# Performance work log

Measured on AMD Instinct MI355X. Metric: run time of the kernel, lower is better.

The kernel has to match this reference:

```python
import jax, jax.numpy as jnp
import numpy as np

N, E = 50000, 800000
IN = OUT = 128
T, R, H = 4, 6, 8
DK = OUT // H


def setup_inputs() -> dict:
    key = jax.random.key(0)
    ks = iter(jax.random.split(key, 24))
    nk = lambda: next(ks)
    return {
        "node_inp": jax.random.normal(nk(), (N, IN), jnp.float32),
        "node_type": jax.random.randint(nk(), (N,), 0, T),
        "edge_index": jax.random.randint(nk(), (2, E), 0, N),
        "edge_type": jax.random.randint(nk(), (E,), 0, R),
        "edge_sign": jax.random.randint(nk(), (E,), -2, 2),
        "edge_distance": jax.random.uniform(nk(), (E,), jnp.float32, 0.0, 2e5),
        "Wq": jax.random.normal(nk(), (T, IN, OUT), jnp.float32) / np.float32(np.sqrt(IN)),
        "bq": jnp.zeros((T, OUT), jnp.float32),
        "Wk": jax.random.normal(nk(), (T, IN, OUT), jnp.float32) / np.float32(np.sqrt(IN)),
        "bk": jnp.zeros((T, OUT), jnp.float32),
        "Wv": jax.random.normal(nk(), (T, IN, OUT), jnp.float32) / np.float32(np.sqrt(IN)),
        "bv": jnp.zeros((T, OUT), jnp.float32),
        "rel_q": jax.random.normal(nk(), (R, H, DK), jnp.float32) * 0.2,
        "rel_k": jax.random.normal(nk(), (R, H, DK), jnp.float32) * 0.2,
        "rel_v": jax.random.normal(nk(), (R, H, DK), jnp.float32) * 0.2,
        "sign_k_neutral": jnp.ones((H, DK), jnp.float32),
        "sign_v_neutral": jnp.ones((H, DK), jnp.float32),
        "rel_bias": jnp.zeros((R, H), jnp.float32),
        "dist_alpha": jnp.asarray(0.5, jnp.float32),
        "dist_tau": jnp.asarray(100000.0, jnp.float32),
        "skip": jnp.ones((T,), jnp.float32),
        "ln_gamma": jnp.ones((T, OUT), jnp.float32),
        "ln_beta": jnp.zeros((T, OUT), jnp.float32),
    }


def reference(node_inp, node_type, edge_index, edge_type, edge_sign, edge_distance,
              Wq, bq, Wk, bk, Wv, bv, rel_q, rel_k, rel_v,
              sign_k_neutral, sign_v_neutral, rel_bias, dist_alpha, dist_tau,
              skip, ln_gamma, ln_beta):
    n = node_inp.shape[0]
    src, dst = edge_index[0], edge_index[1]

    # edge_sign normalization: anything < -1 or == 0 -> -2 (neutral), else clamp to {-1, 1}
    es = jnp.where((edge_sign < -1) | (edge_sign == 0), -2, jnp.clip(edge_sign, -1, 1))
    sign_idx = jnp.where(es == -1, 0, jnp.where(es == 1, 1, 2))  # [E]

    # per-type Q/K/V projections, then select by node_type
    idx = jnp.arange(n)
    Q = (jnp.einsum('ni,tio->tno', node_inp, Wq) + bq[:, None, :])[node_type, idx]
    K = (jnp.einsum('ni,tio->tno', node_inp, Wk) + bk[:, None, :])[node_type, idx]
    V = (jnp.einsum('ni,tio->tno', node_inp, Wv) + bv[:, None, :])[node_type, idx]
    Q = Q.reshape(n, H, DK); K = K.reshape(n, H, DK); V = V.reshape(n, H, DK)

    sign_k_all = jnp.concatenate([-jnp.ones((1, H, DK), Q.dtype), jnp.ones((1, H, DK), Q.dtype), sign_k_neutral[None]], 0)
    sign_v_all = jnp.concatenate([-jnp.ones((1, H, DK), Q.dtype), jnp.ones((1, H, DK), Q.dtype), sign_v_neutral[None]], 0)

    q_eff = Q[dst] * rel_q[edge_type]                        # [E,H,DK]
    k_eff = K[src] * rel_k[edge_type] * sign_k_all[sign_idx]  # [E,H,DK]
    v_eff = V[src] * rel_v[edge_type] * sign_v_all[sign_idx]  # [E,H,DK]

    scores = (q_eff * k_eff).sum(-1) / np.float32(np.sqrt(DK))  # [E,H]
    scores = scores + rel_bias[edge_type]
    phi = dist_alpha * jnp.exp(-edge_distance / (dist_tau + 1e-9))
    scores = scores + phi[:, None]

    # destination-grouped softmax over edges
    m = jax.ops.segment_max(scores, dst, num_segments=n)      # [N,H]
    ex = jnp.exp(scores - m[dst])
    Z = jax.ops.segment_sum(ex, dst, num_segments=n)          # [N,H]
    attn = ex / (Z[dst] + 1e-9)                               # [E,H]

    msg = (v_eff * attn[..., None]).reshape(-1, OUT)          # [E,OUT]
    out = jax.ops.segment_sum(msg, dst, num_segments=n)       # [N,OUT]

    alpha = jax.nn.sigmoid(skip)[node_type][:, None]          # [N,1]
    mix = alpha * out + (1.0 - alpha) * node_inp
    mu = mix.mean(-1, keepdims=True)
    var = ((mix - mu) ** 2).mean(-1, keepdims=True)
    normed = (mix - mu) / jnp.sqrt(var + 1e-5)
    return normed * ln_gamma[node_type] + ln_beta[node_type]
```

## Files before the change

### kernel.cpp

```cpp
#include <hip/hip_runtime.h>

#define N_NODES 50000
#define N_EDGES 800000
#define DIM 128
#define NT 4
#define NR 6
#define NH 8
#define NBLK_SCAN ((N_NODES + 255) / 256)
#define NBLK2 ((N_NODES + 1023) / 1024)
#define NTILE_ROW 3129
#define NPAD_MAX (NTILE_ROW * 16)

#define XCVT_N (N_NODES * DIM / 4)
#define WT_N   (NT * 3 * DIM * DIM)
#define WCB_N  (24 * 32)
#define PREP_TOTAL (XCVT_N + WT_N + WCB_N)
#define PREP_BLOCKS ((PREP_TOTAL + 255) / 256)
#define HIST_BLOCKS (N_EDGES / 256)
#define A_PREP_BASE NBLK_SCAN
#define A_HIST_BASE (NBLK_SCAN + PREP_BLOCKS)
#define A_BLOCKS (A_HIST_BASE + HIST_BLOCKS)

#define D_BLOCKS 4693

typedef __attribute__((ext_vector_type(8))) short bf16x8;
typedef __attribute__((ext_vector_type(4))) float f32x4;

__device__ __forceinline__ unsigned short f2bf(float f) {
    unsigned int u = __float_as_uint(f);
    return (unsigned short)((u + 0x7fffu + ((u >> 16) & 1u)) >> 16);
}
__device__ __forceinline__ float blo(unsigned int u) { return __uint_as_float(u << 16); }
__device__ __forceinline__ float bhi(unsigned int u) { return __uint_as_float(u & 0xffff0000u); }

__device__ __forceinline__ int sign_index(int s) {
    if (s < -1 || s == 0) return 2;
    return (s == -1) ? 0 : 1;
}

__global__ __launch_bounds__(256) void k_A(
    const int* __restrict__ ntype, int* __restrict__ bhist, int* __restrict__ opad,
    const float* __restrict__ x,
    const float* __restrict__ Wq, const float* __restrict__ Wk, const float* __restrict__ Wv,
    const float* __restrict__ rel_q, const float* __restrict__ rel_k,
    const float* __restrict__ rel_v,
    const float* __restrict__ skn, const float* __restrict__ svn,
    unsigned short* __restrict__ xb, unsigned short* __restrict__ Wt,
    uint4* __restrict__ wcb,
    const int* __restrict__ ei, int* __restrict__ cnt, int* __restrict__ posw)
{
    int blk = blockIdx.x;
    if (blk < NBLK_SCAN) {
        __shared__ int h[NT];
        if (threadIdx.x < NT) h[threadIdx.x] = 0;
        __syncthreads();
        int n = blk * 256 + threadIdx.x;
        if (n < N_NODES) atomicAdd(&h[ntype[n]], 1);
        if (n < NPAD_MAX) opad[n] = -1;
        __syncthreads();
        if (threadIdx.x < NT) bhist[blk * NT + threadIdx.x] = h[threadIdx.x];
        return;
    }
    if (blk < A_HIST_BASE) {
        int i = (blk - A_PREP_BASE) * 256 + threadIdx.x;
        if (i < XCVT_N) {
            float4 v = ((const float4*)x)[i];
            ushort4 o;
            o.x = f2bf(v.x); o.y = f2bf(v.y); o.z = f2bf(v.z); o.w = f2bf(v.w);
            ((ushort4*)xb)[i] = o;
        } else if (i < XCVT_N + WT_N) {
            int j = i - XCVT_N;
            int in = j & 127;
            int b2 = j >> 7;
            int out = b2 & 127;
            int ts = b2 >> 7;
            int sel = ts % 3, t = ts / 3;
            const float* W = sel == 0 ? Wq : (sel == 1 ? Wk : Wv);
            Wt[j] = f2bf(W[((size_t)t * DIM + in) * DIM + out]);
        } else if (i < PREP_TOTAL) {
            int j = i - XCVT_N - WT_N;
            int p = j & 31;
            int cmb = j >> 5;
            int et = cmb & 7, sidx = cmb >> 3;
            if (et < NR) {
                int h2 = p >> 2;
                unsigned d[4];
                #pragma unroll
                for (int q = 0; q < 4; ++q) {
                    int o = 4 * p + q;
                    int rb = (et * NH + h2) * 16 + (o & 15);
                    float sgk = sidx == 0 ? -1.f : (sidx == 1 ? 1.f : skn[o]);
                    float sgv = sidx == 0 ? -1.f : (sidx == 1 ? 1.f : svn[o]);
                    float wk = rel_q[rb] * rel_k[rb] * sgk * 0.25f;
                    float wv = rel_v[rb] * sgv;
                    d[q] = (unsigned)f2bf(wk) | ((unsigned)f2bf(wv) << 16);
                }
                uint4 u; u.x = d[0]; u.y = d[1]; u.z = d[2]; u.w = d[3];
                wcb[cmb * 32 + p] = u;
            }
        }
        return;
    }
    int e = (blk - A_HIST_BASE) * 256 + threadIdx.x;
    if (e < N_EDGES) posw[e] = atomicAdd(&cnt[ei[N_EDGES + e]], 1);
}

__global__ __launch_bounds__(1024) void k_B(
    const int* __restrict__ bhist, int* __restrict__ bbase, int* __restrict__ pb_g,
    const int* __restrict__ cnt, int* __restrict__ offs, int* __restrict__ bsum)
{
    int tid = threadIdx.x;
    if (blockIdx.x == 0) {
        __shared__ int s[1024];
        __shared__ int pb[NT + 1];
        int t = tid / NBLK_SCAN;
        int b = tid - t * NBLK_SCAN;
        int v = (tid < NT * NBLK_SCAN) ? bhist[b * NT + t] : 0;
        s[tid] = v;
        __syncthreads();
        for (int d = 1; d < 1024; d <<= 1) {
            int add = (tid >= d) ? s[tid - d] : 0;
            __syncthreads();
            s[tid] += add;
            __syncthreads();
        }
        if (tid == 0) {
            int acc = 0;
            for (int tt = 0; tt < NT; ++tt) {
                pb[tt] = acc;
                int tot = s[(tt + 1) * NBLK_SCAN - 1] - (tt ? s[tt * NBLK_SCAN - 1] : 0);
                acc += ((tot + 15) >> 4) << 4;
            }
            pb[NT] = acc;
        }
        __syncthreads();
        if (tid < NT * NBLK_SCAN) {
            int excl = s[tid] - v;
            int base_t = t ? s[t * NBLK_SCAN - 1] : 0;
            bbase[b * NT + t] = pb[t] + (excl - base_t);
        }
        if (tid <= NT) pb_g[tid] = pb[tid];
        return;
    }
    int sb = blockIdx.x - 1;
    __shared__ int s[1024];
    int i = sb * 1024 + tid;
    int v = (i < N_NODES) ? cnt[i] : 0;
    s[tid] = v;
    __syncthreads();
    for (int d = 1; d < 1024; d <<= 1) {
        int add = (tid >= d) ? s[tid - d] : 0;
        __syncthreads();
        s[tid] += add;
        __syncthreads();
    }
    if (i < N_NODES) offs[i] = s[tid] - v;
    if (tid == 1023) bsum[sb] = s[1023];
}

__global__ __launch_bounds__(256) void k_C(
    const int* __restrict__ ntype, const int* __restrict__ bbase, int* __restrict__ order_pad,
    int* __restrict__ slot,
    const int* __restrict__ bsum, int* __restrict__ bofs, int* __restrict__ offs)
{
    int blk = blockIdx.x;
    if (blk < NBLK_SCAN) {
        __shared__ int cur[NT];
        if (threadIdx.x < NT) cur[threadIdx.x] = bbase[blk * NT + threadIdx.x];
        __syncthreads();
        int n = blk * 256 + threadIdx.x;
        if (n < N_NODES) {
            int t = ntype[n];
            int pos = atomicAdd(&cur[t], 1);
            order_pad[pos] = n;
            slot[n] = pos;
        }
        return;
    }
    __shared__ int s[256];
    int t = threadIdx.x;
    int v = (t < NBLK2) ? bsum[t] : 0;
    s[t] = v;
    __syncthreads();
    for (int d = 1; d < 256; d <<= 1) {
        int add = (t >= d) ? s[t - d] : 0;
        __syncthreads();
        s[t] += add;
        __syncthreads();
    }
    if (t < NBLK2) {
        int b = s[t] - v;
        bofs[t] = b;
        if (t == NBLK2 - 1) offs[N_NODES] = N_EDGES - b;
    }
}

__global__ __launch_bounds__(256) void k_D(
    const unsigned short* __restrict__ xb, const unsigned short* __restrict__ Wt,
    const int* __restrict__ order_pad, const int* __restrict__ pb_g,
    const float* __restrict__ bq, const float* __restrict__ bk, const float* __restrict__ bv,
    float* __restrict__ Qf, unsigned int* __restrict__ KVu,
    const int* __restrict__ slot,
    const int* __restrict__ ei, const int* __restrict__ etype,
    const int* __restrict__ esign, const float* __restrict__ edist,
    const float* __restrict__ dalpha, const float* __restrict__ dtau,
    const int* __restrict__ offs, const int* __restrict__ bofs,
    const int* __restrict__ posw, int2* __restrict__ edata)
{
    int b = blockIdx.x;
    int d3 = b / 3, m = b - d3 * 3;
    if (m == 2) {
        int e0 = d3 * 512 + threadIdx.x;
        if (e0 >= N_EDGES) return;
        int e1 = e0 + 256;
        bool v1 = (e1 < N_EDGES);
        int dst0 = ei[N_EDGES + e0];
        int src0 = ei[e0];
        int dst1 = v1 ? ei[N_EDGES + e1] : 0;
        int src1 = v1 ? ei[e1] : 0;
        int pw0 = posw[e0];
        int pw1 = v1 ? posw[e1] : 0;
        int sl0 = slot[src0];
        int sl1 = slot[src1];
        int of0 = offs[dst0] + bofs[dst0 >> 10];
        int of1 = offs[dst1] + bofs[dst1 >> 10];
        int cmb0 = sign_index(esign[e0]) * 8 + etype[e0];
        int cmb1 = v1 ? (sign_index(esign[e1]) * 8 + etype[e1]) : 0;
        float rtau = 1.f / (dtau[0] + 1e-9f);
        float da = dalpha[0];
        float phi0 = da * __expf(-edist[e0] * rtau);
        float phi1 = da * __expf(-(v1 ? edist[e1] : 0.f) * rtau);
        edata[of0 + pw0] = make_int2(sl0 | (cmb0 << 16), __float_as_int(phi0));
        if (v1) edata[of1 + pw1] = make_int2(sl1 | (cmb1 << 16), __float_as_int(phi1));
        return;
    }
    int tile = d3 * 2 + m;
    if (tile >= NTILE_ROW) return;
    int row0 = tile * 16;
    if (row0 >= pb_g[NT]) return;
    int t = (row0 >= pb_g[3]) ? 3 : (row0 >= pb_g[2]) ? 2 : (row0 >= pb_g[1]) ? 1 : 0;
    int wave = threadIdx.x >> 6, lane = threadIdx.x & 63;
    int col = wave * 16 + (lane & 15);
    int arow = row0 + (lane & 15);
    int nidA = order_pad[arow];
    const unsigned short* xrow = xb + (size_t)(nidA < 0 ? 0 : nidA) * DIM;
    int ko = (lane >> 4) * 8;
    bf16x8 afrag[4];
    #pragma unroll
    for (int kt = 0; kt < 4; ++kt) afrag[kt] = *(const bf16x8*)(xrow + kt * 32 + ko);

    #pragma unroll
    for (int g = 0; g < 2; ++g) {
        int wcol = g * 64 + col;
        const unsigned short* wrow = Wt + ((size_t)(t * 3 + 0) * DIM + wcol) * DIM;
        f32x4 acc = {0.f, 0.f, 0.f, 0.f};
        #pragma unroll
        for (int kt = 0; kt < 4; ++kt) {
            bf16x8 bfr = *(const bf16x8*)(wrow + kt * 32 + ko);
            acc = __builtin_amdgcn_mfma_f32_16x16x32_bf16(afrag[kt], bfr, acc, 0, 0, 0);
        }
        float bias = bq[t * DIM + wcol];
        #pragma unroll
        for (int r = 0; r < 4; ++r) {
            int lrow = (lane >> 4) * 4 + r;
            Qf[(size_t)(row0 + lrow) * DIM + wcol] = acc[r] + bias;
        }
    }
    #pragma unroll
    for (int g = 0; g < 2; ++g) {
        int wcol = g * 64 + col;
        const unsigned short* wrowK = Wt + ((size_t)(t * 3 + 1) * DIM + wcol) * DIM;
        const unsigned short* wrowV = Wt + ((size_t)(t * 3 + 2) * DIM + wcol) * DIM;
        f32x4 accK = {0.f, 0.f, 0.f, 0.f};
        f32x4 accV = {0.f, 0.f, 0.f, 0.f};
        #pragma unroll
        for (int kt = 0; kt < 4; ++kt) {
            bf16x8 bK = *(const bf16x8*)(wrowK + kt * 32 + ko);
            bf16x8 bV = *(const bf16x8*)(wrowV + kt * 32 + ko);
            accK = __builtin_amdgcn_mfma_f32_16x16x32_bf16(afrag[kt], bK, accK, 0, 0, 0);
            accV = __builtin_amdgcn_mfma_f32_16x16x32_bf16(afrag[kt], bV, accV, 0, 0, 0);
        }
        float bk_ = bk[t * DIM + wcol], bv_ = bv[t * DIM + wcol];
        #pragma unroll
        for (int r = 0; r < 4; ++r) {
            int lrow = (lane >> 4) * 4 + r;
            unsigned d = (unsigned)f2bf(accK[r] + bk_) | ((unsigned)f2bf(accV[r] + bv_) << 16);
            KVu[(size_t)(row0 + lrow) * DIM + wcol] = d;
        }
    }
}

__global__ __launch_bounds__(256) void k_attn(
    const float4* __restrict__ Qf4, const uint4* __restrict__ KV,
    const uint4* __restrict__ WCB,
    const float* __restrict__ x, const int* __restrict__ ntype,
    const int* __restrict__ slot,
    const int* __restrict__ offs, const int* __restrict__ bofs,
    const int2* __restrict__ edata,
    const float* __restrict__ rbias, const float* __restrict__ skip,
    const float* __restrict__ gmm, const float* __restrict__ bta,
    float* __restrict__ out)
{
    __shared__ float rb_s[NR * NH];
    if (threadIdx.x < NR * NH) rb_s[threadIdx.x] = rbias[threadIdx.x];
    __syncthreads();
    const int wave = threadIdx.x >> 6, lane = threadIdx.x & 63;
    const int n = blockIdx.x * 4 + wave;
    const int p = lane & 31;
    const int hi = lane >> 5;
    const int h = p >> 2;
    const int beg = offs[n] + bofs[n >> 10];
    const int end = offs[n + 1] + bofs[(n + 1) >> 10];

    const int sl = slot[n];
    const float4 q4 = Qf4[(size_t)sl * 32 + p];

    float Z = 0.f, a0 = 0.f, a1 = 0.f, a2 = 0.f, a3 = 0.f;

    auto process = [&](int2 r) {
        int src = r.x & 0xffff;
        unsigned cmb = ((unsigned)r.x) >> 16;
        uint4 kv = KV[(size_t)src * 32 + p];
        uint4 w = WCB[cmb * 32 + p];
        float pp = (q4.x * blo(w.x)) * blo(kv.x);
        pp = fmaf(q4.y * blo(w.y), blo(kv.y), pp);
        pp = fmaf(q4.z * blo(w.z), blo(kv.z), pp);
        pp = fmaf(q4.w * blo(w.w), blo(kv.w), pp);
        pp += __shfl_xor(pp, 1, 4);
        pp += __shfl_xor(pp, 2, 4);
        float ex = __expf(pp + rb_s[(cmb & 7) * NH + h] + __int_as_float(r.y));
        Z += ex;
        a0 = fmaf(bhi(kv.x) * bhi(w.x), ex, a0);
        a1 = fmaf(bhi(kv.y) * bhi(w.y), ex, a1);
        a2 = fmaf(bhi(kv.z) * bhi(w.z), ex, a2);
        a3 = fmaf(bhi(kv.w) * bhi(w.w), ex, a3);
    };

    int rem = end - beg;
    int j = beg;
    if (rem >= 4) {
        int2 r0 = edata[j + hi];
        int2 r1 = edata[j + 2 + hi];
        while (true) {
            int2 c0 = r0, c1 = r1;
            j += 4; rem -= 4;
            if (rem >= 4) { r0 = edata[j + hi]; r1 = edata[j + 2 + hi]; }
            process(c0);
            process(c1);
            if (rem < 4) break;
        }
    }
    while (rem >= 2) {
        int2 c = edata[j + hi];
        process(c);
        j += 2; rem -= 2;
    }
    if (rem) {
        int2 r = edata[j];
        int src = r.x & 0xffff;
        unsigned cmb = ((unsigned)r.x) >> 16;
        uint4 kv = KV[(size_t)src * 32 + p];
        uint4 w = WCB[cmb * 32 + p];
        float pp = (q4.x * blo(w.x)) * blo(kv.x);
        pp = fmaf(q4.y * blo(w.y), blo(kv.y), pp);
        pp = fmaf(q4.z * blo(w.z), blo(kv.z), pp);
        pp = fmaf(q4.w * blo(w.w), blo(kv.w), pp);
        pp += __shfl_xor(pp, 1, 4);
        pp += __shfl_xor(pp, 2, 4);
        float ex = __expf(pp + rb_s[(cmb & 7) * NH + h] + __int_as_float(r.y));
        ex = hi ? 0.f : ex;
        Z += ex;
        a0 = fmaf(bhi(kv.x) * bhi(w.x), ex, a0);
        a1 = fmaf(bhi(kv.y) * bhi(w.y), ex, a1);
        a2 = fmaf(bhi(kv.z) * bhi(w.z), ex, a2);
        a3 = fmaf(bhi(kv.w) * bhi(w.w), ex, a3);
    }

    Z  += __shfl_xor(Z, 32, 64);
    a0 += __shfl_xor(a0, 32, 64);
    a1 += __shfl_xor(a1, 32, 64);
    a2 += __shfl_xor(a2, 32, 64);
    a3 += __shfl_xor(a3, 32, 64);

    float rz = 1.f / (Z + 1e-9f);
    int t = ntype[n];
    float alpha = 1.f / (1.f + __expf(-skip[t]));
    float4 x4 = ((const float4*)x)[(size_t)n * 32 + p];
    float m0 = fmaf(alpha, a0 * rz - x4.x, x4.x);
    float m1 = fmaf(alpha, a1 * rz - x4.y, x4.y);
    float m2 = fmaf(alpha, a2 * rz - x4.z, x4.z);
    float m3 = fmaf(alpha, a3 * rz - x4.w, x4.w);

    float s = (m0 + m1) + (m2 + m3);
    float s2 = fmaf(m0, m0, m1 * m1) + fmaf(m2, m2, m3 * m3);
    #pragma unroll
    for (int d = 32; d >= 1; d >>= 1) {
        s += __shfl_xor(s, d, 64);
        s2 += __shfl_xor(s2, d, 64);
    }
    float mu = s * (1.f / (2 * DIM));
    float var = s2 * (1.f / (2 * DIM)) - mu * mu;
    float rstd = rsqrtf(var + 1e-5f);
    if (hi == 0) {
        float4 g4 = ((const float4*)gmm)[t * 32 + p];
        float4 b4 = ((const float4*)bta)[t * 32 + p];
        float4 o4;
        o4.x = (m0 - mu) * rstd * g4.x + b4.x;
        o4.y = (m1 - mu) * rstd * g4.y + b4.y;
        o4.z = (m2 - mu) * rstd * g4.z + b4.z;
        o4.w = (m3 - mu) * rstd * g4.w + b4.w;
        ((float4*)out)[(size_t)n * 32 + p] = o4;
    }
}

extern "C" void kernel_launch(void* const* d_in, const int* in_sizes, int n_in,
                              void* d_out, int out_size, void* d_ws, size_t ws_size,
                              hipStream_t stream) {
    const float* x      = (const float*)d_in[0];
    const int*   ntype  = (const int*)d_in[1];
    const int*   ei     = (const int*)d_in[2];
    const int*   etype  = (const int*)d_in[3];
    const int*   esign  = (const int*)d_in[4];
    const float* edist  = (const float*)d_in[5];
    const float* Wq     = (const float*)d_in[6];
    const float* bq     = (const float*)d_in[7];
    const float* Wk     = (const float*)d_in[8];
    const float* bk     = (const float*)d_in[9];
    const float* Wv     = (const float*)d_in[10];
    const float* bv     = (const float*)d_in[11];
    const float* rel_q  = (const float*)d_in[12];
    const float* rel_k  = (const float*)d_in[13];
    const float* rel_v  = (const float*)d_in[14];
    const float* skn    = (const float*)d_in[15];
    const float* svn    = (const float*)d_in[16];
    const float* rbias  = (const float*)d_in[17];
    const float* dalpha = (const float*)d_in[18];
    const float* dtau   = (const float*)d_in[19];
    const float* skip   = (const float*)d_in[20];
    const float* gmm    = (const float*)d_in[21];
    const float* bta    = (const float*)d_in[22];
    float* out = (float*)d_out;

    char* ws = (char*)d_ws;
    float*          Qf     = (float*)         (ws + 0);
    unsigned int*   KVu    = (unsigned int*)  (ws + 25632768);
    unsigned short* xb     = (unsigned short*)(ws + 51265536);
    unsigned short* Wt     = (unsigned short*)(ws + 64065536);
    uint4*          wcb    = (uint4*)         (ws + 64458752);
    int*            cnt    = (int*)           (ws + 64471040);
    int*            offs   = (int*)           (ws + 64672256);
    int*            bsum   = (int*)           (ws + 64873472);
    int*            bofs   = (int*)           (ws + 64873984);
    int*            posw   = (int*)           (ws + 64874496);
    int2*           edata  = (int2*)          (ws + 68074496);
    int*            opad   = (int*)           (ws + 74475008);
    int*            slot   = (int*)           (ws + 74675712);
    int*            bhist  = (int*)           (ws + 74876416);
    int*            bbase  = (int*)           (ws + 74880512);
    int*            pb     = (int*)           (ws + 74884608);

    hipMemsetAsync(cnt, 0, (size_t)N_NODES * 4, stream);
    k_A <<<A_BLOCKS, 256, 0, stream>>>(ntype, bhist, opad,
                                       x, Wq, Wk, Wv, rel_q, rel_k, rel_v, skn, svn,
                                       xb, Wt, wcb, ei, cnt, posw);
    k_B <<<1 + NBLK2, 1024, 0, stream>>>(bhist, bbase, pb, cnt, offs, bsum);
    k_C <<<NBLK_SCAN + 1, 256, 0, stream>>>(ntype, bbase, opad, slot, bsum, bofs, offs);
    k_D <<<D_BLOCKS, 256, 0, stream>>>(xb, Wt, opad, pb, bq, bk, bv,
                                       Qf, KVu, slot,
                                       ei, etype, esign, edist, dalpha, dtau,
                                       offs, bofs, posw, edata);
    k_attn <<<N_NODES / 4, 256, 0, stream>>>((const float4*)Qf, (const uint4*)KVu,
                                             (const uint4*)wcb, x, ntype, slot, offs, bofs,
                                             edata, rbias, skip, gmm, bta, out);
}
```

Baseline: 184.5 us.

## Split fused projection/edge-emit kernel and process four row tiles per block

Separates the combined kernel into an edge-emit kernel and a projection kernel launched back to back. The projection kernel now handles four 16-row tiles per block and reloads weight fragments only when the node type changes, cutting repeated weight loads. Edge records are written as single 64-bit nontemporal stores. The cost is an extra launch, lost overlap between emit and projection work within one grid, and higher register pressure from holding four tiles of A fragments.

```diff
diff --git a/kernel.cpp b/kernel.cpp
--- a/kernel.cpp
+++ b/kernel.cpp
@@ -21,7 +21,9 @@
 #define A_HIST_BASE (NBLK_SCAN + PREP_BLOCKS)
 #define A_BLOCKS (A_HIST_BASE + HIST_BLOCKS)
 
-#define D_BLOCKS 4693
+#define PCHUNK 4
+#define PROJ_BLOCKS ((NTILE_ROW + PCHUNK - 1) / PCHUNK)
+#define EMIT_BLOCKS ((N_EDGES + 511) / 512)
 
 typedef __attribute__((ext_vector_type(8))) short bf16x8;
 typedef __attribute__((ext_vector_type(4))) float f32x4;
@@ -195,11 +197,7 @@
     }
 }
 
-__global__ __launch_bounds__(256) void k_D(
-    const unsigned short* __restrict__ xb, const unsigned short* __restrict__ Wt,
-    const int* __restrict__ order_pad, const int* __restrict__ pb_g,
-    const float* __restrict__ bq, const float* __restrict__ bk, const float* __restrict__ bv,
-    float* __restrict__ Qf, unsigned int* __restrict__ KVu,
+__global__ __launch_bounds__(256) void k_emit(
     const int* __restrict__ slot,
     const int* __restrict__ ei, const int* __restrict__ etype,
     const int* __restrict__ esign, const float* __restrict__ edist,
@@ -207,85 +205,132 @@
     const int* __restrict__ offs, const int* __restrict__ bofs,
     const int* __restrict__ posw, int2* __restrict__ edata)
 {
-    int b = blockIdx.x;
-    int d3 = b / 3, m = b - d3 * 3;
-    if (m == 2) {
-        int e0 = d3 * 512 + threadIdx.x;
-        if (e0 >= N_EDGES) return;
-        int e1 = e0 + 256;
-        bool v1 = (e1 < N_EDGES);
-        int dst0 = ei[N_EDGES + e0];
-        int src0 = ei[e0];
-        int dst1 = v1 ? ei[N_EDGES + e1] : 0;
-        int src1 = v1 ? ei[e1] : 0;
-        int pw0 = posw[e0];
-        int pw1 = v1 ? posw[e1] : 0;
-        int sl0 = slot[src0];
-        int sl1 = slot[src1];
-        int of0 = offs[dst0] + bofs[dst0 >> 10];
-        int of1 = offs[dst1] + bofs[dst1 >> 10];
-        int cmb0 = sign_index(esign[e0]) * 8 + etype[e0];
-        int cmb1 = v1 ? (sign_index(esign[e1]) * 8 + etype[e1]) : 0;
-        float rtau = 1.f / (dtau[0] + 1e-9f);
-        float da = dalpha[0];
-        float phi0 = da * __expf(-edist[e0] * rtau);
-        float phi1 = da * __expf(-(v1 ? edist[e1] : 0.f) * rtau);
-        edata[of0 + pw0] = make_int2(sl0 | (cmb0 << 16), __float_as_int(phi0));
-        if (v1) edata[of1 + pw1] = make_int2(sl1 | (cmb1 << 16), __float_as_int(phi1));
-        return;
-    }
-    int tile = d3 * 2 + m;
-    if (tile >= NTILE_ROW) return;
-    int row0 = tile * 16;
-    if (row0 >= pb_g[NT]) return;
-    int t = (row0 >= pb_g[3]) ? 3 : (row0 >= pb_g[2]) ? 2 : (row0 >= pb_g[1]) ? 1 : 0;
-    int wave = threadIdx.x >> 6, lane = threadIdx.x & 63;
-    int col = wave * 16 + (lane & 15);
-    int arow = row0 + (lane & 15);
-    int nidA = order_pad[arow];
-    const unsigned short* xrow = xb + (size_t)(nidA < 0 ? 0 : nidA) * DIM;
-    int ko = (lane >> 4) * 8;
-    bf16x8 afrag[4];
+    int e0 = blockIdx.x * 512 + threadIdx.x;
+    if (e0 >= N_EDGES) return;
+    int e1 = e0 + 256;
+    bool v1 = (e1 < N_EDGES);
+    int dst0 = ei[N_EDGES + e0];
+    int src0 = ei[e0];
+    int dst1 = v1 ? ei[N_EDGES + e1] : 0;
+    int src1 = v1 ? ei[e1] : 0;
+    int pw0 = posw[e0];
+    int pw1 = v1 ? posw[e1] : 0;
+    int sl0 = slot[src0];
+    int sl1 = slot[src1];
+    int of0 = offs[dst0] + bofs[dst0 >> 10];
+    int of1 = offs[dst1] + bofs[dst1 >> 10];
+    int cmb0 = sign_index(esign[e0]) * 8 + etype[e0];
+    int cmb1 = v1 ? (sign_index(esign[e1]) * 8 + etype[e1]) : 0;
+    float rtau = 1.f / (dtau[0] + 1e-9f);
+    float da = dalpha[0];
+    float phi0 = da * __expf(-edist[e0] * rtau);
+    float phi1 = da * __expf(-(v1 ? edist[e1] : 0.f) * rtau);
+    long long p0 = ((long long)(unsigned)__float_as_int(phi0) << 32)
+                 | (unsigned)(sl0 | (cmb0 << 16));
+    __builtin_nontemporal_store(p0, (long long*)(edata + of0 + pw0));
+    if (v1) {
+        long long p1 = ((long long)(unsigned)__float_as_int(phi1) << 32)
+                     | (unsigned)(sl1 | (cmb1 << 16));
+        __builtin_nontemporal_store(p1, (long long*)(edata + of1 + pw1));
+    }
+}
+
+__global__ __launch_bounds__(256) void k_projm(
+    const unsigned short* __restrict__ xb, const unsigned short* __restrict__ Wt,
+    const int* __restrict__ order_pad, const int* __restrict__ pb_g,
+    const float* __restrict__ bq, const float* __restrict__ bk, const float* __restrict__ bv,
+    float* __restrict__ Qf, unsigned int* __restrict__ KVu)
+{
+    const int chunk = blockIdx.x;
+    const int wave = threadIdx.x >> 6, lane = threadIdx.x & 63;
+    const int col = wave * 16 + (lane & 15);
+    const int ko = (lane >> 4) * 8;
+    const int tmax = pb_g[NT];
+    const int pb1 = pb_g[1], pb2 = pb_g[2], pb3 = pb_g[3];
+
+    bf16x8 afrag[PCHUNK][4];
+    int row0s[PCHUNK];
+    bool valid[PCHUNK];
     #pragma unroll
-    for (int kt = 0; kt < 4; ++kt) afrag[kt] = *(const bf16x8*)(xrow + kt * 32 + ko);
+    for (int tt = 0; tt < PCHUNK; ++tt) {
+        int tile = chunk * PCHUNK + tt;
+        int row0 = tile * 16;
+        row0s[tt] = row0;
+        bool v = (tile < NTILE_ROW) && (row0 < tmax);
+        valid[tt] = v;
+        int arow = row0 + (lane & 15);
+        int nidA = v ? order_pad[arow] : -1;
+        const unsigned short* xrow = xb + (size_t)(nidA < 0 ? 0 : nidA) * DIM;
+        #pragma unroll
+        for (int kt = 0; kt < 4; ++kt)
+            afrag[tt][kt] = *(const bf16x8*)(xrow + kt * 32 + ko);
+    }
 
     #pragma unroll
     for (int g = 0; g < 2; ++g) {
         int wcol = g * 64 + col;
-        const unsigned short* wrow = Wt + ((size_t)(t * 3 + 0) * DIM + wcol) * DIM;
-        f32x4 acc = {0.f, 0.f, 0.f, 0.f};
+        int cur_t = -1;
+        bf16x8 bfr[4];
+        float bias = 0.f;
         #pragma unroll
-        for (int kt = 0; kt < 4; ++kt) {
-            bf16x8 bfr = *(const bf16x8*)(wrow + kt * 32 + ko);
-            acc = __builtin_amdgcn_mfma_f32_16x16x32_bf16(afrag[kt], bfr, acc, 0, 0, 0);
-        }
-        float bias = bq[t * DIM + wcol];
-        #pragma unroll
-        for (int r = 0; r < 4; ++r) {
-            int lrow = (lane >> 4) * 4 + r;
-            Qf[(size_t)(row0 + lrow) * DIM + wcol] = acc[r] + bias;
+        for (int tt = 0; tt < PCHUNK; ++tt) {
+            if (!valid[tt]) continue;
+            int row0 = row0s[tt];
+            int t = (row0 >= pb3) ? 3 : (row0 >= pb2) ? 2 : (row0 >= pb1) ? 1 : 0;
+            if (t != cur_t) {
+                cur_t = t;
+                const unsigned short* wrow = Wt + ((size_t)(t * 3 + 0) * DIM + wcol) * DIM;
+                #pragma unroll
+                for (int kt = 0; kt < 4; ++kt) bfr[kt] = *(const bf16x8*)(wrow + kt * 32 + ko);
+                bias = bq[t * DIM + wcol];
+            }
+            f32x4 acc = {0.f, 0.f, 0.f, 0.f};
+            #pragma unroll
+            for (int kt = 0; kt < 4; ++kt)
+                acc = __builtin_amdgcn_mfma_f32_16x16x32_bf16(afrag[tt][kt], bfr[kt], acc, 0, 0, 0);
+            #pragma unroll
+            for (int r = 0; r < 4; ++r) {
+                int lrow = (lane >> 4) * 4 + r;
+                Qf[(size_t)(row0 + lrow) * DIM + wcol] = acc[r] + bias;
+            }
         }
     }
     #pragma unroll
     for (int g = 0; g < 2; ++g) {
         int wcol = g * 64 + col;
-        const unsigned short* wrowK = Wt + ((size_t)(t * 3 + 1) * DIM + wcol) * DIM;
-        const unsigned short* wrowV = Wt + ((size_t)(t * 3 + 2) * DIM + wcol) * DIM;
-        f32x4 accK = {0.f, 0.f, 0.f, 0.f};
-        f32x4 accV = {0.f, 0.f, 0.f, 0.f};
+        int cur_t = -1;
+        bf16x8 bK[4], bV[4];
+        float bk_ = 0.f, bv_ = 0.f;
         #pragma unroll
-        for (int kt = 0; kt < 4; ++kt) {
-            bf16x8 bK = *(const bf16x8*)(wrowK + kt * 32 + ko);
-            bf16x8 bV = *(const bf16x8*)(wrowV + kt * 32 + ko);
-            accK = __builtin_amdgcn_mfma_f32_16x16x32_bf16(afrag[kt], bK, accK, 0, 0, 0);
-            accV = __builtin_amdgcn_mfma_f32_16x16x32_bf16(afrag[kt], bV, accV, 0, 0, 0);
-        }
-        float bk_ = bk[t * DIM + wcol], bv_ = bv[t * DIM + wcol];
-        #pragma unroll
-        for (int r = 0; r < 4; ++r) {
-            int lrow = (lane >> 4) * 4 + r;
-            unsigned d = (unsigned)f2bf(accK[r] + bk_) | ((unsigned)f2bf(accV[r] + bv_) << 16);
-            KVu[(size_t)(row0 + lrow) * DIM + wcol] = d;
+        for (int tt = 0; tt < PCHUNK; ++tt) {
+            if (!valid[tt]) continue;
+            int row0 = row0s[tt];
+            int t = (row0 >= pb3) ? 3 : (row0 >= pb2) ? 2 : (row0 >= pb1) ? 1 : 0;
+            if (t != cur_t) {
+                cur_t = t;
+                const unsigned short* wrowK = Wt + ((size_t)(t * 3 + 1) * DIM + wcol) * DIM;
+                const unsigned short* wrowV = Wt + ((size_t)(t * 3 + 2) * DIM + wcol) * DIM;
+                #pragma unroll
+                for (int kt = 0; kt < 4; ++kt) {
+                    bK[kt] = *(const bf16x8*)(wrowK + kt * 32 + ko);
+                    bV[kt] = *(const bf16x8*)(wrowV + kt * 32 + ko);
+                }
+                bk_ = bk[t * DIM + wcol];
+                bv_ = bv[t * DIM + wcol];
+            }
+            f32x4 accK = {0.f, 0.f, 0.f, 0.f};
+            f32x4 accV = {0.f, 0.f, 0.f, 0.f};
+            #pragma unroll
+            for (int kt = 0; kt < 4; ++kt) {
+                accK = __builtin_amdgcn_mfma_f32_16x16x32_bf16(afrag[tt][kt], bK[kt], accK, 0, 0, 0);
+                accV = __builtin_amdgcn_mfma_f32_16x16x32_bf16(afrag[tt][kt], bV[kt], accV, 0, 0, 0);
+            }
+            #pragma unroll
+            for (int r = 0; r < 4; ++r) {
+                int lrow = (lane >> 4) * 4 + r;
+                unsigned d = (unsigned)f2bf(accK[r] + bk_) | ((unsigned)f2bf(accV[r] + bv_) << 16);
+                KVu[(size_t)(row0 + lrow) * DIM + wcol] = d;
+            }
         }
     }
 }
@@ -465,10 +510,9 @@
                                        xb, Wt, wcb, ei, cnt, posw);
     k_B <<<1 + NBLK2, 1024, 0, stream>>>(bhist, bbase, pb, cnt, offs, bsum);
     k_C <<<NBLK_SCAN + 1, 256, 0, stream>>>(ntype, bbase, opad, slot, bsum, bofs, offs);
-    k_D <<<D_BLOCKS, 256, 0, stream>>>(xb, Wt, opad, pb, bq, bk, bv,
-                                       Qf, KVu, slot,
-                                       ei, etype, esign, edist, dalpha, dtau,
-                                       offs, bofs, posw, edata);
+    k_emit <<<EMIT_BLOCKS, 256, 0, stream>>>(slot, ei, etype, esign, edist, dalpha, dtau,
+                                             offs, bofs, posw, edata);
+    k_projm <<<PROJ_BLOCKS, 256, 0, stream>>>(xb, Wt, opad, pb, bq, bk, bv, Qf, KVu);
     k_attn <<<N_NODES / 4, 256, 0, stream>>>((const float4*)Qf, (const uint4*)KVu,
                                              (const uint4*)wcb, x, ntype, slot, offs, bofs,
                                              edata, rbias, skip, gmm, bta, out);
```

Result: no change. 180.9 us (-2.0%).
